# Optimization experiments

Hardware: AMD Instinct MI355X
Metric: run time of the kernel (lower is better)

The kernel has to match this reference:

```python
import jax, jax.numpy as jnp
import numpy as np

B, H, N, D, A = 96, 100, 128, 768, 256  # batch, max_history_num, news_num, news_embedding_dim, attention_dim


def setup_inputs() -> dict:
    key = jax.random.key(0)
    ks = jax.random.split(key, 6)
    w = lambda k, shape: jax.random.normal(k, shape, jnp.float32) * 0.02
    return {
        "history_embedding": jax.random.normal(ks[0], (B, H, D), jnp.float32),
        "candidate_news_representation": jax.random.normal(ks[1], (B, N, D), jnp.float32),
        "W_l": w(ks[2], (D, D)),              # SAGEConv lin_l (neighbor) weight
        "b_l": jnp.zeros((D,), jnp.float32),  # SAGEConv lin_l bias
        "W_r": w(ks[3], (D, D)),              # SAGEConv lin_r (root) weight, bias=False
        "W_K": w(ks[4], (A, D)),              # K Linear, bias=False
        "W_Q": w(ks[5], (A, D)),              # Q Linear, bias=True
        "b_Q": jnp.zeros((A,), jnp.float32),
    }


def reference(history_embedding, candidate_news_representation, W_l, b_l, W_r, W_K, W_Q, b_Q):
    b, h, d = history_embedding.shape
    n = candidate_news_representation.shape[1]
    a_dim = W_K.shape[0]

    # --- GraphSAGE (1 layer SAGEConv, mean aggr, PyG node_dim=-2) ---
    # edge_index: src = user rows 0..b-1 (indexing the history dim!), dst = 0..h-1.
    # Every dst h receives all srcs 0..b-1, so the mean-aggregated neighbor feature is
    # mean over the first b history slots, identical for every h.
    neigh = jnp.mean(history_embedding[:, :b, :], axis=1)  # [b, d]
    gcn = (
        jnp.einsum("bhd,ed->bhe", history_embedding, W_r)
        + (neigh @ W_l.T + b_l)[:, None, :]
    )  # [b, h, d]

    # --- K/Q attention pooling over history ---
    user_rep = gcn[:, 0, :]                                  # [b, d] (gcn_feature[:, :1, :])
    K = jnp.einsum("bhd,ad->bha", gcn, W_K)                  # [b, h, A]
    Q = user_rep @ W_Q.T + b_Q                               # [b, A]
    scores = jnp.einsum("bha,ba->bh", K, Q) / jnp.sqrt(jnp.float32(a_dim))
    alpha = jax.nn.softmax(scores, axis=1)                   # [b, h]
    out = jnp.einsum("bh,bhd->bd", alpha, gcn)               # [b, d]

    # In torch, news_rep/user_rep2 are expand()ed over news_num with identical content,
    # so the per-candidate outputs are all equal: broadcast instead of recomputing.
    return jnp.broadcast_to(out[:, None, :], (b, n, d))
```

## Files before the change

### kernel.cpp

```cpp
#include <hip/hip_runtime.h>
#include <hip/hip_bf16.h>

#define BB 96
#define HH 100
#define NN 128
#define DD 768
#define AA 256

static __device__ __forceinline__ float dot4(float4 a, float4 b) {
  return a.x * b.x + a.y * b.y + a.z * b.z + a.w * b.w;
}

__global__ void k_prep(const float* __restrict__ Wr, const float* __restrict__ WK,
                       const float* __restrict__ hist,
                       float* __restrict__ WrT, float* __restrict__ WKT,
                       float* __restrict__ neigh) {
  __shared__ float tile[32][33];
  int bid = blockIdx.x;
  if (bid < 768) {
    const float* src; float* dst; int R, C, bx, by;
    if (bid < 576) { src = Wr; dst = WrT; R = DD; C = DD; bx = bid % 24; by = bid / 24; }
    else { int id = bid - 576; src = WK; dst = WKT; R = AA; C = DD; bx = id % 24; by = id / 24; }
    int tx = threadIdx.x & 31, ty = threadIdx.x >> 5;
    int c0 = bx * 32, r0 = by * 32;
#pragma unroll
    for (int k = 0; k < 4; ++k)
      tile[ty + 8 * k][tx] = src[(size_t)(r0 + ty + 8 * k) * C + c0 + tx];
    __syncthreads();
#pragma unroll
    for (int k = 0; k < 4; ++k)
      dst[(size_t)(c0 + ty + 8 * k) * R + r0 + tx] = tile[tx][ty + 8 * k];
  } else {
    int b = bid - 768;
    int t = threadIdx.x;
    if (t >= 192) return;
    const float* hb = hist + (size_t)b * HH * DD + t * 4;
    float4 a0 = make_float4(0.f, 0.f, 0.f, 0.f);
    float4 a1 = make_float4(0.f, 0.f, 0.f, 0.f);
#pragma unroll 8
    for (int h = 0; h < 96; h += 2) {
      float4 x = *(const float4*)(hb + (size_t)h * DD);
      float4 y = *(const float4*)(hb + (size_t)(h + 1) * DD);
      a0.x += x.x; a0.y += x.y; a0.z += x.z; a0.w += x.w;
      a1.x += y.x; a1.y += y.y; a1.z += y.z; a1.w += y.w;
    }
    float4 m = make_float4((a0.x + a1.x) * (1.f / 96.f), (a0.y + a1.y) * (1.f / 96.f),
                           (a0.z + a1.z) * (1.f / 96.f), (a0.w + a1.w) * (1.f / 96.f));
    *(float4*)(neigh + (size_t)b * DD + t * 4) = m;
  }
}

__global__ void k_nl_u0(const float* __restrict__ neigh, const float* __restrict__ hist,
                        const float* __restrict__ Wl, const float* __restrict__ bl,
                        const float* __restrict__ Wr,
                        float* __restrict__ nl, float* __restrict__ u0) {
  int e0 = blockIdx.x * 32;
  int b0 = blockIdx.y * 3;
  int lane = threadIdx.x & 63, wave = threadIdx.x >> 6;
  float4 xn[3][3], xh[3][3];
#pragma unroll
  for (int bi = 0; bi < 3; ++bi) {
    int b = b0 + bi;
#pragma unroll
    for (int jj = 0; jj < 3; ++jj) {
      int idx = lane + 64 * jj;
      xn[bi][jj] = ((const float4*)(neigh + (size_t)b * DD))[idx];
      xh[bi][jj] = ((const float4*)(hist + (size_t)b * HH * DD))[idx];
    }
  }
  for (int i = 0; i < 8; ++i) {
    int e = e0 + wave * 8 + i;
    const float4* wl4 = (const float4*)(Wl + (size_t)e * DD);
    const float4* wr4 = (const float4*)(Wr + (size_t)e * DD);
    float pl[3] = {0.f, 0.f, 0.f}, pr[3] = {0.f, 0.f, 0.f};
#pragma unroll
    for (int jj = 0; jj < 3; ++jj) {
      float4 wl = wl4[lane + 64 * jj];
      float4 wr = wr4[lane + 64 * jj];
#pragma unroll
      for (int bi = 0; bi < 3; ++bi) {
        pl[bi] += dot4(wl, xn[bi][jj]);
        pr[bi] += dot4(wr, xh[bi][jj]);
      }
    }
#pragma unroll
    for (int bi = 0; bi < 3; ++bi) {
      float pp = pl[bi], qq = pr[bi];
      for (int off = 32; off; off >>= 1) {
        pp += __shfl_down(pp, off, 64);
        qq += __shfl_down(qq, off, 64);
      }
      if (lane == 0) {
        float nle = pp + bl[e];
        nl[(size_t)(b0 + bi) * DD + e] = nle;
        u0[(size_t)(b0 + bi) * DD + e] = qq + nle;
      }
    }
  }
}

__global__ void k_q(const float* __restrict__ u0, const float* __restrict__ WQ,
                    const float* __restrict__ bQ, float* __restrict__ Qm) {
  int a0 = blockIdx.x * 32;
  int b0 = blockIdx.y * 3;
  int lane = threadIdx.x & 63, wave = threadIdx.x >> 6;
  float4 x[3][3];
#pragma unroll
  for (int bi = 0; bi < 3; ++bi)
#pragma unroll
    for (int jj = 0; jj < 3; ++jj)
      x[bi][jj] = ((const float4*)(u0 + (size_t)(b0 + bi) * DD))[lane + 64 * jj];
  for (int i = 0; i < 8; ++i) {
    int a = a0 + wave * 8 + i;
    const float4* w4 = (const float4*)(WQ + (size_t)a * DD);
    float p[3] = {0.f, 0.f, 0.f};
#pragma unroll
    for (int jj = 0; jj < 3; ++jj) {
      float4 w = w4[lane + 64 * jj];
#pragma unroll
      for (int bi = 0; bi < 3; ++bi) p[bi] += dot4(w, x[bi][jj]);
    }
#pragma unroll
    for (int bi = 0; bi < 3; ++bi) {
      float pp = p[bi];
      for (int off = 32; off; off >>= 1) pp += __shfl_down(pp, off, 64);
      if (lane == 0) Qm[(size_t)(b0 + bi) * AA + a] = pp + bQ[a];
    }
  }
}

__global__ void k_qk(const float* __restrict__ Qm, const float* __restrict__ WKT,
                     float* __restrict__ qk) {
  int d0 = blockIdx.x * 32;
  int b0 = blockIdx.y * 3;
  int lane = threadIdx.x & 63, wave = threadIdx.x >> 6;
  float4 x[3];
#pragma unroll
  for (int bi = 0; bi < 3; ++bi)
    x[bi] = ((const float4*)(Qm + (size_t)(b0 + bi) * AA))[lane];
  for (int i = 0; i < 8; ++i) {
    int d = d0 + wave * 8 + i;
    float4 w = ((const float4*)(WKT + (size_t)d * AA))[lane];
    float p[3];
#pragma unroll
    for (int bi = 0; bi < 3; ++bi) p[bi] = dot4(w, x[bi]);
#pragma unroll
    for (int bi = 0; bi < 3; ++bi) {
      float pp = p[bi];
      for (int off = 32; off; off >>= 1) pp += __shfl_down(pp, off, 64);
      if (lane == 0) qk[(size_t)(b0 + bi) * DD + d] = pp;
    }
  }
}

__global__ void k_v(const float* __restrict__ qk, const float* __restrict__ WrT,
                    float* __restrict__ vv) {
  int d0 = blockIdx.x * 32;
  int b0 = blockIdx.y * 3;
  int lane = threadIdx.x & 63, wave = threadIdx.x >> 6;
  float4 x[3][3];
#pragma unroll
  for (int bi = 0; bi < 3; ++bi)
#pragma unroll
    for (int jj = 0; jj < 3; ++jj)
      x[bi][jj] = ((const float4*)(qk + (size_t)(b0 + bi) * DD))[lane + 64 * jj];
  for (int i = 0; i < 8; ++i) {
    int d = d0 + wave * 8 + i;
    const float4* w4 = (const float4*)(WrT + (size_t)d * DD);
    float p[3] = {0.f, 0.f, 0.f};
#pragma unroll
    for (int jj = 0; jj < 3; ++jj) {
      float4 w = w4[lane + 64 * jj];
#pragma unroll
      for (int bi = 0; bi < 3; ++bi) p[bi] += dot4(w, x[bi][jj]);
    }
#pragma unroll
    for (int bi = 0; bi < 3; ++bi) {
      float pp = p[bi];
      for (int off = 32; off; off >>= 1) pp += __shfl_down(pp, off, 64);
      if (lane == 0) vv[(size_t)(b0 + bi) * DD + d] = pp * (1.f / 16.f);
    }
  }
}

__global__ void k_scores(const float* __restrict__ hist, const float* __restrict__ vv,
                         float* __restrict__ sc) {
  int b = blockIdx.x, hg = blockIdx.y;
  int lane = threadIdx.x & 63, wave = threadIdx.x >> 6;
  float4 v[3];
  const float4* vb = (const float4*)(vv + (size_t)b * DD);
#pragma unroll
  for (int jj = 0; jj < 3; ++jj) v[jj] = vb[lane + 64 * jj];
  const float* hb = hist + (size_t)b * HH * DD;
  for (int i = 0; i < 5; ++i) {
    int h = hg * 20 + wave * 5 + i;
    const float4* r = (const float4*)(hb + (size_t)h * DD);
    float p = 0.f;
#pragma unroll
    for (int jj = 0; jj < 3; ++jj) p += dot4(r[lane + 64 * jj], v[jj]);
    for (int off = 32; off; off >>= 1) p += __shfl_down(p, off, 64);
    if (lane == 0) sc[b * 128 + h] = p;
  }
}

__global__ void k_wsum(const float* __restrict__ hist, const float* __restrict__ sc,
                       float* __restrict__ wsum) {
  int b = blockIdx.x;
  int e = blockIdx.y * 256 + threadIdx.x;
  __shared__ float sal[HH];
  __shared__ float s_inv;
  if (threadIdx.x < HH) sal[threadIdx.x] = sc[b * 128 + threadIdx.x];
  __syncthreads();
  if (threadIdx.x == 0) {
    float m = -1e30f;
    for (int h = 0; h < HH; ++h) m = fmaxf(m, sal[h]);
    float s = 0.f;
    for (int h = 0; h < HH; ++h) { float ex = __expf(sal[h] - m); sal[h] = ex; s += ex; }
    s_inv = 1.f / s;
  }
  __syncthreads();
  float inv = s_inv;
  float acc = 0.f;
  const float* hb = hist + (size_t)b * HH * DD + e;
  for (int h = 0; h < HH; h += 4) {
    float v0 = hb[(size_t)(h + 0) * DD];
    float v1 = hb[(size_t)(h + 1) * DD];
    float v2 = hb[(size_t)(h + 2) * DD];
    float v3 = hb[(size_t)(h + 3) * DD];
    acc += sal[h + 0] * v0 + sal[h + 1] * v1 + sal[h + 2] * v2 + sal[h + 3] * v3;
  }
  wsum[(size_t)b * DD + e] = acc * inv;
}

__global__ void k_orow_write(const float* __restrict__ wsum, const float* __restrict__ Wr,
                             const float* __restrict__ nl, float* __restrict__ out) {
  int d0 = blockIdx.x * 32;
  int b0 = blockIdx.y * 3;
  int lane = threadIdx.x & 63, wave = threadIdx.x >> 6;
  __shared__ __align__(16) float s_o[3][32];
  float4 x[3][3];
#pragma unroll
  for (int bi = 0; bi < 3; ++bi)
#pragma unroll
    for (int jj = 0; jj < 3; ++jj)
      x[bi][jj] = ((const float4*)(wsum + (size_t)(b0 + bi) * DD))[lane + 64 * jj];
  for (int i = 0; i < 8; ++i) {
    int d = d0 + wave * 8 + i;
    const float4* w4 = (const float4*)(Wr + (size_t)d * DD);
    float p[3] = {0.f, 0.f, 0.f};
#pragma unroll
    for (int jj = 0; jj < 3; ++jj) {
      float4 w = w4[lane + 64 * jj];
#pragma unroll
      for (int bi = 0; bi < 3; ++bi) p[bi] += dot4(w, x[bi][jj]);
    }
#pragma unroll
    for (int bi = 0; bi < 3; ++bi) {
      float pp = p[bi];
      for (int off = 32; off; off >>= 1) pp += __shfl_down(pp, off, 64);
      if (lane == 0)
        s_o[bi][wave * 8 + i] = pp + nl[(size_t)(b0 + bi) * DD + d];
    }
  }
  __syncthreads();
  float4* out4 = (float4*)out;
  int d4 = d0 >> 2;
#pragma unroll
  for (int k = 0; k < 12; ++k) {
    int g = threadIdx.x + (k << 8);
    int seg = g >> 3, off = g & 7;
    int bi = seg >> 7, n = seg & 127;
    float4 val = *(const float4*)&s_o[bi][off * 4];
    out4[((size_t)(b0 + bi) * NN + n) * (DD / 4) + d4 + off] = val;
  }
}

extern "C" void kernel_launch(void* const* d_in, const int* in_sizes, int n_in,
                              void* d_out, int out_size, void* d_ws, size_t ws_size,
                              hipStream_t stream) {
  const float *hist = nullptr, *Wl = nullptr, *Wr = nullptr, *WK = nullptr,
              *WQ = nullptr, *bl = nullptr, *bQ = nullptr;
  int seenDxD = 0, seenAxD = 0;
  for (int i = 0; i < n_in; ++i) {
    int s = in_sizes[i];
    const float* p = (const float*)d_in[i];
    if (s == BB * HH * DD) hist = p;
    else if (s == BB * NN * DD) {  }
    else if (s == DD * DD) { if (seenDxD++ == 0) Wl = p; else Wr = p; }
    else if (s == AA * DD) { if (seenAxD++ == 0) WK = p; else WQ = p; }
    else if (s == DD) bl = p;
    else if (s == AA) bQ = p;
  }

  float* ws = (float*)d_ws;
  float* WrT   = ws + 0;
  float* WKT   = ws + 589824;
  float* neigh = ws + 786432;
  float* nl    = ws + 860160;
  float* u0    = ws + 933888;
  float* Qm    = ws + 1007616;
  float* qk    = ws + 1032192;
  float* vv    = ws + 1105920;
  float* sc    = ws + 1179648;
  float* wsum  = ws + 1191936;
  float* out = (float*)d_out;

  k_prep      <<<dim3(864),    dim3(256), 0, stream>>>(Wr, WK, hist, WrT, WKT, neigh);
  k_nl_u0     <<<dim3(24, 32), dim3(256), 0, stream>>>(neigh, hist, Wl, bl, Wr, nl, u0);
  k_q         <<<dim3(8, 32),  dim3(256), 0, stream>>>(u0, WQ, bQ, Qm);
  k_qk        <<<dim3(24, 32), dim3(256), 0, stream>>>(Qm, WKT, qk);
  k_v         <<<dim3(24, 32), dim3(256), 0, stream>>>(qk, WrT, vv);
  k_scores    <<<dim3(96, 5),  dim3(256), 0, stream>>>(hist, vv, sc);
  k_wsum      <<<dim3(96, 3),  dim3(256), 0, stream>>>(hist, sc, wsum);
  k_orow_write<<<dim3(24, 32), dim3(256), 0, stream>>>(wsum, Wr, nl, out);
}
```

Before: 95.31 us.

## Fuse eight phase kernels into one cooperative persistent kernel with grid syncs

Turns each of the eight stage kernels into a device function and runs them all inside one cooperative kernel. A grid-stride loop covers each phase's work units and grid.sync separates the phases. The goal is to remove the launch overhead and inter-kernel gaps of eight small launches. In exchange it adds grid-wide barrier cost, limits the grid to what can be co-resident, and keeps the separate kernels as a fallback if the cooperative launch fails.

```diff
diff --git a/kernel.cpp b/kernel.cpp
--- a/kernel.cpp
+++ b/kernel.cpp
@@ -1,5 +1,8 @@
 #include <hip/hip_runtime.h>
+#include <hip/hip_cooperative_groups.h>
 #include <hip/hip_bf16.h>
+
+namespace cg = cooperative_groups;
 
 #define BB 96
 #define HH 100
@@ -11,17 +14,17 @@
   return a.x * b.x + a.y * b.y + a.z * b.z + a.w * b.w;
 }
 
-__global__ void k_prep(const float* __restrict__ Wr, const float* __restrict__ WK,
-                       const float* __restrict__ hist,
-                       float* __restrict__ WrT, float* __restrict__ WKT,
-                       float* __restrict__ neigh) {
-  __shared__ float tile[32][33];
-  int bid = blockIdx.x;
-  if (bid < 768) {
+
+static __device__ void phase_prep(int u, int tid,
+                                  const float* __restrict__ Wr, const float* __restrict__ WK,
+                                  const float* __restrict__ hist,
+                                  float* __restrict__ WrT, float* __restrict__ WKT,
+                                  float* __restrict__ neigh, float (*tile)[33]) {
+  if (u < 768) {
     const float* src; float* dst; int R, C, bx, by;
-    if (bid < 576) { src = Wr; dst = WrT; R = DD; C = DD; bx = bid % 24; by = bid / 24; }
-    else { int id = bid - 576; src = WK; dst = WKT; R = AA; C = DD; bx = id % 24; by = id / 24; }
-    int tx = threadIdx.x & 31, ty = threadIdx.x >> 5;
+    if (u < 576) { src = Wr; dst = WrT; R = DD; C = DD; bx = u % 24; by = u / 24; }
+    else { int id = u - 576; src = WK; dst = WKT; R = AA; C = DD; bx = id % 24; by = id / 24; }
+    int tx = tid & 31, ty = tid >> 5;
     int c0 = bx * 32, r0 = by * 32;
 #pragma unroll
     for (int k = 0; k < 4; ++k)
@@ -30,33 +33,36 @@
 #pragma unroll
     for (int k = 0; k < 4; ++k)
       dst[(size_t)(c0 + ty + 8 * k) * R + r0 + tx] = tile[tx][ty + 8 * k];
+    __syncthreads();
   } else {
-    int b = bid - 768;
-    int t = threadIdx.x;
-    if (t >= 192) return;
-    const float* hb = hist + (size_t)b * HH * DD + t * 4;
-    float4 a0 = make_float4(0.f, 0.f, 0.f, 0.f);
-    float4 a1 = make_float4(0.f, 0.f, 0.f, 0.f);
+    int b = u - 768;
+    if (tid < 192) {
+      const float* hb = hist + (size_t)b * HH * DD + tid * 4;
+      float4 a0 = make_float4(0.f, 0.f, 0.f, 0.f);
+      float4 a1 = make_float4(0.f, 0.f, 0.f, 0.f);
 #pragma unroll 8
-    for (int h = 0; h < 96; h += 2) {
-      float4 x = *(const float4*)(hb + (size_t)h * DD);
-      float4 y = *(const float4*)(hb + (size_t)(h + 1) * DD);
-      a0.x += x.x; a0.y += x.y; a0.z += x.z; a0.w += x.w;
-      a1.x += y.x; a1.y += y.y; a1.z += y.z; a1.w += y.w;
-    }
-    float4 m = make_float4((a0.x + a1.x) * (1.f / 96.f), (a0.y + a1.y) * (1.f / 96.f),
-                           (a0.z + a1.z) * (1.f / 96.f), (a0.w + a1.w) * (1.f / 96.f));
-    *(float4*)(neigh + (size_t)b * DD + t * 4) = m;
-  }
-}
-
-__global__ void k_nl_u0(const float* __restrict__ neigh, const float* __restrict__ hist,
-                        const float* __restrict__ Wl, const float* __restrict__ bl,
-                        const float* __restrict__ Wr,
-                        float* __restrict__ nl, float* __restrict__ u0) {
-  int e0 = blockIdx.x * 32;
-  int b0 = blockIdx.y * 3;
-  int lane = threadIdx.x & 63, wave = threadIdx.x >> 6;
+      for (int h = 0; h < 96; h += 2) {
+        float4 x = *(const float4*)(hb + (size_t)h * DD);
+        float4 y = *(const float4*)(hb + (size_t)(h + 1) * DD);
+        a0.x += x.x; a0.y += x.y; a0.z += x.z; a0.w += x.w;
+        a1.x += y.x; a1.y += y.y; a1.z += y.z; a1.w += y.w;
+      }
+      float4 m = make_float4((a0.x + a1.x) * (1.f / 96.f), (a0.y + a1.y) * (1.f / 96.f),
+                             (a0.z + a1.z) * (1.f / 96.f), (a0.w + a1.w) * (1.f / 96.f));
+      *(float4*)(neigh + (size_t)b * DD + tid * 4) = m;
+    }
+    __syncthreads();
+  }
+}
+
+static __device__ void phase_nlu0(int u, int tid,
+                                  const float* __restrict__ neigh, const float* __restrict__ hist,
+                                  const float* __restrict__ Wl, const float* __restrict__ bl,
+                                  const float* __restrict__ Wr,
+                                  float* __restrict__ nl, float* __restrict__ u0) {
+  int e0 = (u % 24) * 32;
+  int b0 = (u / 24) * 3;
+  int lane = tid & 63, wave = tid >> 6;
   float4 xn[3][3], xh[3][3];
 #pragma unroll
   for (int bi = 0; bi < 3; ++bi) {
@@ -99,11 +105,12 @@
   }
 }
 
-__global__ void k_q(const float* __restrict__ u0, const float* __restrict__ WQ,
-                    const float* __restrict__ bQ, float* __restrict__ Qm) {
-  int a0 = blockIdx.x * 32;
-  int b0 = blockIdx.y * 3;
-  int lane = threadIdx.x & 63, wave = threadIdx.x >> 6;
+static __device__ void phase_q(int u, int tid,
+                               const float* __restrict__ u0, const float* __restrict__ WQ,
+                               const float* __restrict__ bQ, float* __restrict__ Qm) {
+  int a0 = (u % 8) * 32;
+  int b0 = (u / 8) * 3;
+  int lane = tid & 63, wave = tid >> 6;
   float4 x[3][3];
 #pragma unroll
   for (int bi = 0; bi < 3; ++bi)
@@ -129,11 +136,12 @@
   }
 }
 
-__global__ void k_qk(const float* __restrict__ Qm, const float* __restrict__ WKT,
-                     float* __restrict__ qk) {
-  int d0 = blockIdx.x * 32;
-  int b0 = blockIdx.y * 3;
-  int lane = threadIdx.x & 63, wave = threadIdx.x >> 6;
+static __device__ void phase_qk(int u, int tid,
+                                const float* __restrict__ Qm, const float* __restrict__ WKT,
+                                float* __restrict__ qk) {
+  int d0 = (u % 24) * 32;
+  int b0 = (u / 24) * 3;
+  int lane = tid & 63, wave = tid >> 6;
   float4 x[3];
 #pragma unroll
   for (int bi = 0; bi < 3; ++bi)
@@ -153,11 +161,12 @@
   }
 }
 
-__global__ void k_v(const float* __restrict__ qk, const float* __restrict__ WrT,
-                    float* __restrict__ vv) {
-  int d0 = blockIdx.x * 32;
-  int b0 = blockIdx.y * 3;
-  int lane = threadIdx.x & 63, wave = threadIdx.x >> 6;
+static __device__ void phase_v(int u, int tid,
+                               const float* __restrict__ qk, const float* __restrict__ WrT,
+                               float* __restrict__ vv) {
+  int d0 = (u % 24) * 32;
+  int b0 = (u / 24) * 3;
+  int lane = tid & 63, wave = tid >> 6;
   float4 x[3][3];
 #pragma unroll
   for (int bi = 0; bi < 3; ++bi)
@@ -183,10 +192,11 @@
   }
 }
 
-__global__ void k_scores(const float* __restrict__ hist, const float* __restrict__ vv,
-                         float* __restrict__ sc) {
-  int b = blockIdx.x, hg = blockIdx.y;
-  int lane = threadIdx.x & 63, wave = threadIdx.x >> 6;
+static __device__ void phase_scores(int u, int tid,
+                                    const float* __restrict__ hist, const float* __restrict__ vv,
+                                    float* __restrict__ sc) {
+  int b = u % 96, hg = u / 96;
+  int lane = tid & 63, wave = tid >> 6;
   float4 v[3];
   const float4* vb = (const float4*)(vv + (size_t)b * DD);
 #pragma unroll
@@ -203,23 +213,22 @@
   }
 }
 
-__global__ void k_wsum(const float* __restrict__ hist, const float* __restrict__ sc,
-                       float* __restrict__ wsum) {
-  int b = blockIdx.x;
-  int e = blockIdx.y * 256 + threadIdx.x;
-  __shared__ float sal[HH];
-  __shared__ float s_inv;
-  if (threadIdx.x < HH) sal[threadIdx.x] = sc[b * 128 + threadIdx.x];
+static __device__ void phase_wsum(int u, int tid,
+                                  const float* __restrict__ hist, const float* __restrict__ sc,
+                                  float* __restrict__ wsum, float* sal) {
+  int b = u % 96;
+  int e = (u / 96) * 256 + tid;
+  if (tid < HH) sal[tid] = sc[b * 128 + tid];
   __syncthreads();
-  if (threadIdx.x == 0) {
+  if (tid == 0) {
     float m = -1e30f;
     for (int h = 0; h < HH; ++h) m = fmaxf(m, sal[h]);
     float s = 0.f;
     for (int h = 0; h < HH; ++h) { float ex = __expf(sal[h] - m); sal[h] = ex; s += ex; }
-    s_inv = 1.f / s;
+    sal[100] = 1.f / s;
   }
   __syncthreads();
-  float inv = s_inv;
+  float inv = sal[100];
   float acc = 0.f;
   const float* hb = hist + (size_t)b * HH * DD + e;
   for (int h = 0; h < HH; h += 4) {
@@ -230,14 +239,16 @@
     acc += sal[h + 0] * v0 + sal[h + 1] * v1 + sal[h + 2] * v2 + sal[h + 3] * v3;
   }
   wsum[(size_t)b * DD + e] = acc * inv;
-}
-
-__global__ void k_orow_write(const float* __restrict__ wsum, const float* __restrict__ Wr,
-                             const float* __restrict__ nl, float* __restrict__ out) {
-  int d0 = blockIdx.x * 32;
-  int b0 = blockIdx.y * 3;
-  int lane = threadIdx.x & 63, wave = threadIdx.x >> 6;
-  __shared__ __align__(16) float s_o[3][32];
+  __syncthreads();
+}
+
+static __device__ void phase_orow(int u, int tid,
+                                  const float* __restrict__ wsum, const float* __restrict__ Wr,
+                                  const float* __restrict__ nl, float* __restrict__ out,
+                                  float* sal) {
+  int d0 = (u % 24) * 32;
+  int b0 = (u / 24) * 3;
+  int lane = tid & 63, wave = tid >> 6;
   float4 x[3][3];
 #pragma unroll
   for (int bi = 0; bi < 3; ++bi)
@@ -259,7 +270,7 @@
       float pp = p[bi];
       for (int off = 32; off; off >>= 1) pp += __shfl_down(pp, off, 64);
       if (lane == 0)
-        s_o[bi][wave * 8 + i] = pp + nl[(size_t)(b0 + bi) * DD + d];
+        sal[bi * 32 + wave * 8 + i] = pp + nl[(size_t)(b0 + bi) * DD + d];
     }
   }
   __syncthreads();
@@ -267,12 +278,85 @@
   int d4 = d0 >> 2;
 #pragma unroll
   for (int k = 0; k < 12; ++k) {
-    int g = threadIdx.x + (k << 8);
+    int g = tid + (k << 8);
     int seg = g >> 3, off = g & 7;
     int bi = seg >> 7, n = seg & 127;
-    float4 val = *(const float4*)&s_o[bi][off * 4];
+    float4 val = *(const float4*)&sal[bi * 32 + off * 4];
     out4[((size_t)(b0 + bi) * NN + n) * (DD / 4) + d4 + off] = val;
   }
+  __syncthreads();
+}
+
+__global__ void __launch_bounds__(256, 3)
+mega(const float* __restrict__ hist, const float* __restrict__ Wl,
+     const float* __restrict__ bl, const float* __restrict__ Wr,
+     const float* __restrict__ WK, const float* __restrict__ WQ,
+     const float* __restrict__ bQ,
+     float* __restrict__ WrT, float* __restrict__ WKT, float* __restrict__ neigh,
+     float* __restrict__ nl, float* __restrict__ u0, float* __restrict__ Qm,
+     float* __restrict__ qk, float* __restrict__ vv, float* __restrict__ sc,
+     float* __restrict__ wsum, float* __restrict__ out) {
+  cg::grid_group grid = cg::this_grid();
+  __shared__ __align__(16) float tile[32][33];
+  __shared__ __align__(16) float sal[112];
+  int tid = threadIdx.x;
+  for (int u = blockIdx.x; u < 864; u += gridDim.x)
+    phase_prep(u, tid, Wr, WK, hist, WrT, WKT, neigh, tile);
+  grid.sync();
+  for (int u = blockIdx.x; u < 768; u += gridDim.x)
+    phase_nlu0(u, tid, neigh, hist, Wl, bl, Wr, nl, u0);
+  grid.sync();
+  for (int u = blockIdx.x; u < 256; u += gridDim.x)
+    phase_q(u, tid, u0, WQ, bQ, Qm);
+  grid.sync();
+  for (int u = blockIdx.x; u < 768; u += gridDim.x)
+    phase_qk(u, tid, Qm, WKT, qk);
+  grid.sync();
+  for (int u = blockIdx.x; u < 768; u += gridDim.x)
+    phase_v(u, tid, qk, WrT, vv);
+  grid.sync();
+  for (int u = blockIdx.x; u < 480; u += gridDim.x)
+    phase_scores(u, tid, hist, vv, sc);
+  grid.sync();
+  for (int u = blockIdx.x; u < 288; u += gridDim.x)
+    phase_wsum(u, tid, hist, sc, wsum, sal);
+  grid.sync();
+  for (int u = blockIdx.x; u < 768; u += gridDim.x)
+    phase_orow(u, tid, wsum, Wr, nl, out, sal);
+}
+
+__global__ void __launch_bounds__(256) f_prep(const float* Wr, const float* WK,
+                                              const float* hist, float* WrT, float* WKT,
+                                              float* neigh) {
+  __shared__ __align__(16) float tile[32][33];
+  phase_prep(blockIdx.x, threadIdx.x, Wr, WK, hist, WrT, WKT, neigh, tile);
+}
+__global__ void __launch_bounds__(256) f_nlu0(const float* neigh, const float* hist,
+                                              const float* Wl, const float* bl,
+                                              const float* Wr, float* nl, float* u0) {
+  phase_nlu0(blockIdx.x, threadIdx.x, neigh, hist, Wl, bl, Wr, nl, u0);
+}
+__global__ void __launch_bounds__(256) f_q(const float* u0, const float* WQ,
+                                           const float* bQ, float* Qm) {
+  phase_q(blockIdx.x, threadIdx.x, u0, WQ, bQ, Qm);
+}
+__global__ void __launch_bounds__(256) f_qk(const float* Qm, const float* WKT, float* qk) {
+  phase_qk(blockIdx.x, threadIdx.x, Qm, WKT, qk);
+}
+__global__ void __launch_bounds__(256) f_v(const float* qk, const float* WrT, float* vv) {
+  phase_v(blockIdx.x, threadIdx.x, qk, WrT, vv);
+}
+__global__ void __launch_bounds__(256) f_scores(const float* hist, const float* vv, float* sc) {
+  phase_scores(blockIdx.x, threadIdx.x, hist, vv, sc);
+}
+__global__ void __launch_bounds__(256) f_wsum(const float* hist, const float* sc, float* wsum) {
+  __shared__ __align__(16) float sal[112];
+  phase_wsum(blockIdx.x, threadIdx.x, hist, sc, wsum, sal);
+}
+__global__ void __launch_bounds__(256) f_orow(const float* wsum, const float* Wr,
+                                              const float* nl, float* out) {
+  __shared__ __align__(16) float sal[112];
+  phase_orow(blockIdx.x, threadIdx.x, wsum, Wr, nl, out, sal);
 }
 
 extern "C" void kernel_launch(void* const* d_in, const int* in_sizes, int n_in,
@@ -297,20 +381,38 @@
   float* WKT   = ws + 589824;
   float* neigh = ws + 786432;
   float* nl    = ws + 860160;
-  float* u0    = ws + 933888;
+  float* u0v   = ws + 933888;
   float* Qm    = ws + 1007616;
   float* qk    = ws + 1032192;
   float* vv    = ws + 1105920;
   float* sc    = ws + 1179648;
-  float* wsum  = ws + 1191936;
-  float* out = (float*)d_out;
-
-  k_prep      <<<dim3(864),    dim3(256), 0, stream>>>(Wr, WK, hist, WrT, WKT, neigh);
-  k_nl_u0     <<<dim3(24, 32), dim3(256), 0, stream>>>(neigh, hist, Wl, bl, Wr, nl, u0);
-  k_q         <<<dim3(8, 32),  dim3(256), 0, stream>>>(u0, WQ, bQ, Qm);
-  k_qk        <<<dim3(24, 32), dim3(256), 0, stream>>>(Qm, WKT, qk);
-  k_v         <<<dim3(24, 32), dim3(256), 0, stream>>>(qk, WrT, vv);
-  k_scores    <<<dim3(96, 5),  dim3(256), 0, stream>>>(hist, vv, sc);
-  k_wsum      <<<dim3(96, 3),  dim3(256), 0, stream>>>(hist, sc, wsum);
-  k_orow_write<<<dim3(24, 32), dim3(256), 0, stream>>>(wsum, Wr, nl, out);
-}
+  float* wsumv = ws + 1191936;
+  float* outp  = (float*)d_out;
+
+  int maxPerCU = 0;
+  hipError_t qerr = hipOccupancyMaxActiveBlocksPerMultiprocessor(&maxPerCU, mega, 256, 0);
+  int grid = 768;
+  if (qerr == hipSuccess && maxPerCU >= 1) {
+    int cap = maxPerCU * 256;
+    if (cap < grid) grid = cap;
+  } else {
+    grid = 512;
+  }
+
+  void* args[] = {(void*)&hist, (void*)&Wl, (void*)&bl, (void*)&Wr, (void*)&WK,
+                  (void*)&WQ, (void*)&bQ, (void*)&WrT, (void*)&WKT, (void*)&neigh,
+                  (void*)&nl, (void*)&u0v, (void*)&Qm, (void*)&qk, (void*)&vv,
+                  (void*)&sc, (void*)&wsumv, (void*)&outp};
+  hipError_t lerr = hipLaunchCooperativeKernel((const void*)mega, dim3(grid), dim3(256),
+                                               args, 0, stream);
+  if (lerr != hipSuccess) {
+    f_prep  <<<dim3(864), dim3(256), 0, stream>>>(Wr, WK, hist, WrT, WKT, neigh);
+    f_nlu0  <<<dim3(768), dim3(256), 0, stream>>>(neigh, hist, Wl, bl, Wr, nl, u0v);
+    f_q     <<<dim3(256), dim3(256), 0, stream>>>(u0v, WQ, bQ, Qm);
+    f_qk    <<<dim3(768), dim3(256), 0, stream>>>(Qm, WKT, qk);
+    f_v     <<<dim3(768), dim3(256), 0, stream>>>(qk, WrT, vv);
+    f_scores<<<dim3(480), dim3(256), 0, stream>>>(hist, vv, sc);
+    f_wsum  <<<dim3(288), dim3(256), 0, stream>>>(hist, sc, wsumv);
+    f_orow  <<<dim3(768), dim3(256), 0, stream>>>(wsumv, Wr, nl, outp);
+  }
+}
```

Measured after the change: 355.9 us. +273.4%, slower.

## Precompute Wr^T·WK^T weight product and fuse scoring, softmax, weighted sum

Applied to the files above, without the earlier changes.

Instead of transposing Wr and WK and then applying them one after another per batch (Q→WK→Wr), k_prep now computes the combined product M = (WK·Wr)^T once, so each batch needs one 256-wide matvec to get the score vector. The separate score and weighted-sum kernels are merged into one k_attn kernel that computes scores in shared memory, does a wave-level softmax and then the weighted sum. This removes two launches and the qk/sc round trips through memory. In exchange, the 768x768x256 weight product is recomputed on every call with a simple shared-memory tiled loop, and each of the 3 column-slice blocks per batch recomputes all 100 scores, tripling the history reads for scoring.

```diff
diff --git a/kernel.cpp b/kernel.cpp
--- a/kernel.cpp
+++ b/kernel.cpp
@@ -11,42 +11,54 @@
   return a.x * b.x + a.y * b.y + a.z * b.z + a.w * b.w;
 }
 
-__global__ void k_prep(const float* __restrict__ Wr, const float* __restrict__ WK,
-                       const float* __restrict__ hist,
-                       float* __restrict__ WrT, float* __restrict__ WKT,
-                       float* __restrict__ neigh) {
-  __shared__ float tile[32][33];
+__global__ void __launch_bounds__(256)
+k_prep(const float* __restrict__ Wr, const float* __restrict__ WK,
+       const float* __restrict__ hist,
+       float* __restrict__ MT, float* __restrict__ neigh) {
+  __shared__ float sWr[32][33];
+  __shared__ float sWK[32][33];
   int bid = blockIdx.x;
-  if (bid < 768) {
-    const float* src; float* dst; int R, C, bx, by;
-    if (bid < 576) { src = Wr; dst = WrT; R = DD; C = DD; bx = bid % 24; by = bid / 24; }
-    else { int id = bid - 576; src = WK; dst = WKT; R = AA; C = DD; bx = id % 24; by = id / 24; }
-    int tx = threadIdx.x & 31, ty = threadIdx.x >> 5;
-    int c0 = bx * 32, r0 = by * 32;
+  int tid = threadIdx.x;
+  if (bid < 192) {
+    int d0 = (bid % 24) * 32;
+    int a0 = (bid / 24) * 32;
+    int tx = tid & 31, ty = tid >> 5;
+    float acc[4] = {0.f, 0.f, 0.f, 0.f};
+    for (int e0 = 0; e0 < DD; e0 += 32) {
+#pragma unroll
+      for (int k = 0; k < 4; ++k) {
+        sWr[ty + 8 * k][tx] = Wr[(size_t)(e0 + ty + 8 * k) * DD + d0 + tx];
+        sWK[ty + 8 * k][tx] = WK[(size_t)(a0 + ty + 8 * k) * DD + e0 + tx];
+      }
+      __syncthreads();
+#pragma unroll 8
+      for (int e = 0; e < 32; ++e) {
+        float w = sWr[e][tx];
+#pragma unroll
+        for (int k = 0; k < 4; ++k) acc[k] += w * sWK[ty + 8 * k][e];
+      }
+      __syncthreads();
+    }
 #pragma unroll
     for (int k = 0; k < 4; ++k)
-      tile[ty + 8 * k][tx] = src[(size_t)(r0 + ty + 8 * k) * C + c0 + tx];
-    __syncthreads();
-#pragma unroll
-    for (int k = 0; k < 4; ++k)
-      dst[(size_t)(c0 + ty + 8 * k) * R + r0 + tx] = tile[tx][ty + 8 * k];
+      MT[(size_t)(d0 + tx) * AA + a0 + ty + 8 * k] = acc[k];
   } else {
-    int b = bid - 768;
-    int t = threadIdx.x;
-    if (t >= 192) return;
-    const float* hb = hist + (size_t)b * HH * DD + t * 4;
-    float4 a0 = make_float4(0.f, 0.f, 0.f, 0.f);
-    float4 a1 = make_float4(0.f, 0.f, 0.f, 0.f);
+    int b = bid - 192;
+    if (tid < 192) {
+      const float* hb = hist + (size_t)b * HH * DD + tid * 4;
+      float4 a0 = make_float4(0.f, 0.f, 0.f, 0.f);
+      float4 a1 = make_float4(0.f, 0.f, 0.f, 0.f);
 #pragma unroll 8
-    for (int h = 0; h < 96; h += 2) {
-      float4 x = *(const float4*)(hb + (size_t)h * DD);
-      float4 y = *(const float4*)(hb + (size_t)(h + 1) * DD);
-      a0.x += x.x; a0.y += x.y; a0.z += x.z; a0.w += x.w;
-      a1.x += y.x; a1.y += y.y; a1.z += y.z; a1.w += y.w;
-    }
-    float4 m = make_float4((a0.x + a1.x) * (1.f / 96.f), (a0.y + a1.y) * (1.f / 96.f),
-                           (a0.z + a1.z) * (1.f / 96.f), (a0.w + a1.w) * (1.f / 96.f));
-    *(float4*)(neigh + (size_t)b * DD + t * 4) = m;
+      for (int h = 0; h < 96; h += 2) {
+        float4 x = *(const float4*)(hb + (size_t)h * DD);
+        float4 y = *(const float4*)(hb + (size_t)(h + 1) * DD);
+        a0.x += x.x; a0.y += x.y; a0.z += x.z; a0.w += x.w;
+        a1.x += y.x; a1.y += y.y; a1.z += y.z; a1.w += y.w;
+      }
+      float4 m = make_float4((a0.x + a1.x) * (1.f / 96.f), (a0.y + a1.y) * (1.f / 96.f),
+                             (a0.z + a1.z) * (1.f / 96.f), (a0.w + a1.w) * (1.f / 96.f));
+      *(float4*)(neigh + (size_t)b * DD + tid * 4) = m;
+    }
   }
 }
 
@@ -129,8 +141,8 @@
   }
 }
 
-__global__ void k_qk(const float* __restrict__ Qm, const float* __restrict__ WKT,
-                     float* __restrict__ qk) {
+__global__ void k_v(const float* __restrict__ Qm, const float* __restrict__ MT,
+                    float* __restrict__ vv) {
   int d0 = blockIdx.x * 32;
   int b0 = blockIdx.y * 3;
   int lane = threadIdx.x & 63, wave = threadIdx.x >> 6;
@@ -140,40 +152,10 @@
     x[bi] = ((const float4*)(Qm + (size_t)(b0 + bi) * AA))[lane];
   for (int i = 0; i < 8; ++i) {
     int d = d0 + wave * 8 + i;
-    float4 w = ((const float4*)(WKT + (size_t)d * AA))[lane];
+    float4 w = ((const float4*)(MT + (size_t)d * AA))[lane];
     float p[3];
 #pragma unroll
     for (int bi = 0; bi < 3; ++bi) p[bi] = dot4(w, x[bi]);
-#pragma unroll
-    for (int bi = 0; bi < 3; ++bi) {
-      float pp = p[bi];
-      for (int off = 32; off; off >>= 1) pp += __shfl_down(pp, off, 64);
-      if (lane == 0) qk[(size_t)(b0 + bi) * DD + d] = pp;
-    }
-  }
-}
-
-__global__ void k_v(const float* __restrict__ qk, const float* __restrict__ WrT,
-                    float* __restrict__ vv) {
-  int d0 = blockIdx.x * 32;
-  int b0 = blockIdx.y * 3;
-  int lane = threadIdx.x & 63, wave = threadIdx.x >> 6;
-  float4 x[3][3];
-#pragma unroll
-  for (int bi = 0; bi < 3; ++bi)
-#pragma unroll
-    for (int jj = 0; jj < 3; ++jj)
-      x[bi][jj] = ((const float4*)(qk + (size_t)(b0 + bi) * DD))[lane + 64 * jj];
-  for (int i = 0; i < 8; ++i) {
-    int d = d0 + wave * 8 + i;
-    const float4* w4 = (const float4*)(WrT + (size_t)d * DD);
-    float p[3] = {0.f, 0.f, 0.f};
-#pragma unroll
-    for (int jj = 0; jj < 3; ++jj) {
-      float4 w = w4[lane + 64 * jj];
-#pragma unroll
-      for (int bi = 0; bi < 3; ++bi) p[bi] += dot4(w, x[bi][jj]);
-    }
 #pragma unroll
     for (int bi = 0; bi < 3; ++bi) {
       float pp = p[bi];
@@ -183,53 +165,58 @@
   }
 }
 
-__global__ void k_scores(const float* __restrict__ hist, const float* __restrict__ vv,
-                         float* __restrict__ sc) {
-  int b = blockIdx.x, hg = blockIdx.y;
-  int lane = threadIdx.x & 63, wave = threadIdx.x >> 6;
-  float4 v[3];
-  const float4* vb = (const float4*)(vv + (size_t)b * DD);
-#pragma unroll
-  for (int jj = 0; jj < 3; ++jj) v[jj] = vb[lane + 64 * jj];
-  const float* hb = hist + (size_t)b * HH * DD;
-  for (int i = 0; i < 5; ++i) {
-    int h = hg * 20 + wave * 5 + i;
-    const float4* r = (const float4*)(hb + (size_t)h * DD);
-    float p = 0.f;
-#pragma unroll
-    for (int jj = 0; jj < 3; ++jj) p += dot4(r[lane + 64 * jj], v[jj]);
-    for (int off = 32; off; off >>= 1) p += __shfl_down(p, off, 64);
-    if (lane == 0) sc[b * 128 + h] = p;
-  }
-}
-
-__global__ void k_wsum(const float* __restrict__ hist, const float* __restrict__ sc,
-                       float* __restrict__ wsum) {
+__global__ void __launch_bounds__(256)
+k_attn(const float* __restrict__ hist, const float* __restrict__ vv,
+       float* __restrict__ wsum) {
   int b = blockIdx.x;
-  int e = blockIdx.y * 256 + threadIdx.x;
+  int es = blockIdx.y;
+  int tid = threadIdx.x, lane = tid & 63, wave = tid >> 6;
+  __shared__ __align__(16) float sv[DD];
   __shared__ float sal[HH];
-  __shared__ float s_inv;
-  if (threadIdx.x < HH) sal[threadIdx.x] = sc[b * 128 + threadIdx.x];
-  __syncthreads();
-  if (threadIdx.x == 0) {
-    float m = -1e30f;
-    for (int h = 0; h < HH; ++h) m = fmaxf(m, sal[h]);
-    float s = 0.f;
-    for (int h = 0; h < HH; ++h) { float ex = __expf(sal[h] - m); sal[h] = ex; s += ex; }
-    s_inv = 1.f / s;
-  }
-  __syncthreads();
-  float inv = s_inv;
-  float acc = 0.f;
-  const float* hb = hist + (size_t)b * HH * DD + e;
-  for (int h = 0; h < HH; h += 4) {
-    float v0 = hb[(size_t)(h + 0) * DD];
-    float v1 = hb[(size_t)(h + 1) * DD];
-    float v2 = hb[(size_t)(h + 2) * DD];
-    float v3 = hb[(size_t)(h + 3) * DD];
-    acc += sal[h + 0] * v0 + sal[h + 1] * v1 + sal[h + 2] * v2 + sal[h + 3] * v3;
-  }
-  wsum[(size_t)b * DD + e] = acc * inv;
+  if (tid < 192)
+    ((float4*)sv)[tid] = ((const float4*)(vv + (size_t)b * DD))[tid];
+  __syncthreads();
+  {
+    float4 v0 = ((const float4*)sv)[lane];
+    float4 v1 = ((const float4*)sv)[lane + 64];
+    float4 v2 = ((const float4*)sv)[lane + 128];
+    const float* hb = hist + (size_t)b * HH * DD;
+    for (int i = 0; i < 25; ++i) {
+      int h = wave * 25 + i;
+      const float4* r = (const float4*)(hb + (size_t)h * DD);
+      float p = dot4(r[lane], v0) + dot4(r[lane + 64], v1) + dot4(r[lane + 128], v2);
+      for (int off = 32; off; off >>= 1) p += __shfl_down(p, off, 64);
+      if (lane == 0) sal[h] = p;
+    }
+  }
+  __syncthreads();
+  if (wave == 0) {
+    float x0 = (lane < HH) ? sal[lane] : -1e30f;
+    float x1 = (lane + 64 < HH) ? sal[lane + 64] : -1e30f;
+    float m = fmaxf(x0, x1);
+    for (int off = 32; off; off >>= 1) m = fmaxf(m, __shfl_xor(m, off, 64));
+    float e0 = (lane < HH) ? __expf(x0 - m) : 0.f;
+    float e1 = (lane + 64 < HH) ? __expf(x1 - m) : 0.f;
+    float s = e0 + e1;
+    for (int off = 32; off; off >>= 1) s += __shfl_xor(s, off, 64);
+    float inv = 1.f / s;
+    if (lane < HH) sal[lane] = e0 * inv;
+    if (lane + 64 < HH) sal[lane + 64] = e1 * inv;
+  }
+  __syncthreads();
+  {
+    int e = es * 256 + tid;
+    const float* hb = hist + (size_t)b * HH * DD + e;
+    float acc = 0.f;
+    for (int h = 0; h < HH; h += 4) {
+      float v0 = hb[(size_t)(h + 0) * DD];
+      float v1 = hb[(size_t)(h + 1) * DD];
+      float v2 = hb[(size_t)(h + 2) * DD];
+      float v3 = hb[(size_t)(h + 3) * DD];
+      acc += sal[h + 0] * v0 + sal[h + 1] * v1 + sal[h + 2] * v2 + sal[h + 3] * v3;
+    }
+    wsum[(size_t)b * DD + e] = acc;
+  }
 }
 
 __global__ void k_orow_write(const float* __restrict__ wsum, const float* __restrict__ Wr,
@@ -293,24 +280,19 @@
   }
 
   float* ws = (float*)d_ws;
-  float* WrT   = ws + 0;
-  float* WKT   = ws + 589824;
-  float* neigh = ws + 786432;
-  float* nl    = ws + 860160;
-  float* u0    = ws + 933888;
-  float* Qm    = ws + 1007616;
-  float* qk    = ws + 1032192;
-  float* vv    = ws + 1105920;
-  float* sc    = ws + 1179648;
-  float* wsum  = ws + 1191936;
+  float* MT    = ws + 0;
+  float* neigh = ws + 196608;
+  float* nl    = ws + 270336;
+  float* u0    = ws + 344064;
+  float* Qm    = ws + 417792;
+  float* vv    = ws + 442368;
+  float* wsum  = ws + 516096;
   float* out = (float*)d_out;
 
-  k_prep      <<<dim3(864),    dim3(256), 0, stream>>>(Wr, WK, hist, WrT, WKT, neigh);
+  k_prep      <<<dim3(288),    dim3(256), 0, stream>>>(Wr, WK, hist, MT, neigh);
   k_nl_u0     <<<dim3(24, 32), dim3(256), 0, stream>>>(neigh, hist, Wl, bl, Wr, nl, u0);
   k_q         <<<dim3(8, 32),  dim3(256), 0, stream>>>(u0, WQ, bQ, Qm);
-  k_qk        <<<dim3(24, 32), dim3(256), 0, stream>>>(Qm, WKT, qk);
-  k_v         <<<dim3(24, 32), dim3(256), 0, stream>>>(qk, WrT, vv);
-  k_scores    <<<dim3(96, 5),  dim3(256), 0, stream>>>(hist, vv, sc);
-  k_wsum      <<<dim3(96, 3),  dim3(256), 0, stream>>>(hist, sc, wsum);
+  k_v         <<<dim3(24, 32), dim3(256), 0, stream>>>(Qm, MT, vv);
+  k_attn      <<<dim3(96, 3),  dim3(256), 0, stream>>>(hist, vv, wsum);
   k_orow_write<<<dim3(24, 32), dim3(256), 0, stream>>>(wsum, Wr, nl, out);
 }
```

Result: slower. 111.3 us (+16.8%).
